# Performance work log

Measured on AMD Instinct MI355X. Metric: run time of the kernel, lower is better.

Reference implementation:

```python
import jax, jax.numpy as jnp
import numpy as np

B, S, H, NS, HEADS, L = 16, 1024, 1024, 32, 16, 5
DH = H // HEADS
LN_EPS = 1e-7


def setup_inputs() -> dict:
    key = jax.random.key(0)
    ks = jax.random.split(key, 12)
    std = 0.02
    inp = {
        "encoder_layer": jax.random.normal(ks[0], (B, S, H), jnp.float32),
        "lstm_W_ih": jax.random.normal(ks[1], (4 * H, H), jnp.float32) * std,
        "lstm_W_hh": jax.random.normal(ks[2], (4 * H, H), jnp.float32) * std,
        "lstm_b_ih": jnp.zeros((4 * H,), jnp.float32),
        "lstm_b_hh": jnp.zeros((4 * H,), jnp.float32),
        "ln_gamma": jnp.ones((H,), jnp.float32),
        "ln_beta": jnp.zeros((H,), jnp.float32),
        "Wq": jax.random.normal(ks[3], (H, H), jnp.float32) * std,
        "bq": jnp.zeros((H,), jnp.float32),
        "Wk": jax.random.normal(ks[4], (H, H), jnp.float32) * std,
        "bk": jnp.zeros((H,), jnp.float32),
        "Wv": jax.random.normal(ks[5], (H, H), jnp.float32) * std,
        "bv": jnp.zeros((H,), jnp.float32),
        "Wo": jax.random.normal(ks[6], (H, H), jnp.float32) * std,
        "bo": jnp.zeros((H,), jnp.float32),
        "attn_ln_gamma": jnp.ones((H,), jnp.float32),
        "attn_ln_beta": jnp.zeros((H,), jnp.float32),
        "clf_W": jax.random.normal(ks[7], (L, H), jnp.float32) * std,
        "clf_b": jnp.zeros((L,), jnp.float32),
    }
    # contiguous ragged spans: head_j = 32*j, tail_j = 32*(j+1); slice is head+1:tail
    seg = S // NS
    heads = jnp.tile(jnp.arange(NS, dtype=jnp.int32)[None, :] * seg, (B, 1))
    inp["span_head_idxs"] = heads
    inp["span_tail_idxs"] = heads + seg
    inp["span_attention_mask"] = jnp.ones((B, NS), jnp.int32)
    return inp


def _layer_norm(x, gamma, beta):
    mu = jnp.mean(x, axis=-1, keepdims=True)
    var = jnp.mean(jnp.square(x - mu), axis=-1, keepdims=True)
    return (x - mu) * jax.lax.rsqrt(var + LN_EPS) * gamma + beta


def reference(encoder_layer, lstm_W_ih, lstm_W_hh, lstm_b_ih, lstm_b_hh,
              ln_gamma, ln_beta, Wq, bq, Wk, bk, Wv, bv, Wo, bo,
              attn_ln_gamma, attn_ln_beta, clf_W, clf_b,
              span_head_idxs, span_tail_idxs, span_attention_mask):
    # --- unidirectional LSTM over the sequence (torch gate order i,f,g,o) ---
    x_tbh = jnp.swapaxes(encoder_layer, 0, 1)  # [S,B,H]
    h0 = jnp.zeros((B, H), encoder_layer.dtype)
    c0 = jnp.zeros((B, H), encoder_layer.dtype)

    def step(carry, xt):
        h, c = carry
        gates = xt @ lstm_W_ih.T + lstm_b_ih + h @ lstm_W_hh.T + lstm_b_hh
        i, f, g, o = jnp.split(gates, 4, axis=-1)
        i, f, o = jax.nn.sigmoid(i), jax.nn.sigmoid(f), jax.nn.sigmoid(o)
        c = f * c + i * jnp.tanh(g)
        h = o * jnp.tanh(c)
        return (h, c), h

    _, hs = jax.lax.scan(step, (h0, c0), x_tbh)
    enc = jnp.swapaxes(hs, 0, 1)  # [B,S,H]

    # --- ragged span mean pooling (tokens head+1 .. tail-1) via masked matmul ---
    t = jnp.arange(S, dtype=jnp.int32)  # [S]
    span_mask = ((t[None, None, :] >= span_head_idxs[:, :, None] + 1)
                 & (t[None, None, :] < span_tail_idxs[:, :, None]))  # [B,NS,S]
    mf = span_mask.astype(enc.dtype)
    sums = jnp.einsum('bns,bsh->bnh', mf, enc)
    counts = jnp.sum(mf, axis=-1, keepdims=True)
    mean_vec = sums / counts  # [B,NS,H]

    mean_vec = _layer_norm(mean_vec, ln_gamma, ln_beta)

    # --- DeBERTa-style self-attention (relative_attention=False) over spans ---
    m2d = (span_attention_mask[:, None, None, :]
           * span_attention_mask[:, None, :, None])  # [B,1,NS,NS]
    mbool = m2d.astype(bool)

    def split_heads(y):
        return jnp.swapaxes(y.reshape(B, NS, HEADS, DH), 1, 2)  # [B,h,NS,dh]

    q = split_heads(mean_vec @ Wq.T + bq)
    k = split_heads(mean_vec @ Wk.T + bk)
    v = split_heads(mean_vec @ Wv.T + bv)
    scale = jnp.sqrt(jnp.asarray(DH, mean_vec.dtype))
    scores = jnp.einsum('bhqd,bhkd->bhqk', q, k) / scale
    scores = jnp.where(mbool, scores, jnp.finfo(scores.dtype).min)
    probs = jax.nn.softmax(scores, axis=-1)
    probs = jnp.where(mbool, probs, 0.0)  # XSoftmax zeroes masked positions
    ctx = jnp.einsum('bhqk,bhkd->bhqd', probs, v)
    ctx = jnp.swapaxes(ctx, 1, 2).reshape(B, NS, H)
    attn_out = _layer_norm(ctx @ Wo.T + bo + mean_vec, attn_ln_gamma, attn_ln_beta)

    # dropout is identity in eval mode
    logits = attn_out @ clf_W.T + clf_b  # [B,NS,L]
    return logits
```

## Files before the change

kernel.cpp:

```cpp
#include <hip/hip_runtime.h>
#include <hip/hip_bf16.h>

#define DEV __device__ __forceinline__

typedef __attribute__((ext_vector_type(8))) short short8;
typedef __attribute__((ext_vector_type(4))) float f32x4;
typedef __attribute__((ext_vector_type(4))) unsigned int u32x4;

static constexpr int B_ = 16, S_ = 1024, H_ = 1024, NS_ = 32, HEADS_ = 16, L_ = 5;
static constexpr int G4H = 4096;
static constexpr int LSTM_GRID = 64;

DEV unsigned short f2bf(float f){
  union { float f; unsigned int i; } u; u.f = f;
  unsigned int r = (u.i + 0x7fffu + ((u.i >> 16) & 1u)) >> 16;
  return (unsigned short)r;
}
DEV float bf2f(unsigned short h){
  union { unsigned int i; float f; } u; u.i = ((unsigned int)h) << 16;
  return u.f;
}
DEV float sigm(float x){ return 1.f / (1.f + __expf(-x)); }
DEV float tanh_(float x){
  x = fminf(30.f, fmaxf(-30.f, x));
  float e = __expf(-2.f * x);
  return (1.f - e) / (1.f + e);
}

DEV u32x4 load_coh16(const void* p){
  u32x4 r;
  asm volatile("global_load_dwordx4 %0, %1, off sc0 sc1" : "=v"(r) : "v"(p));
  return r;
}
DEV void store_coh16(void* p, u32x4 v){
  asm volatile("global_store_dwordx4 %0, %1, off sc0 sc1" :: "v"(p), "v"(v) : "memory");
}

__global__ void k_spanof(const int* __restrict__ head, const int* __restrict__ tail,
                         int* __restrict__ spanof){
  const int b = blockIdx.x;
  for (int t = threadIdx.x; t < S_; t += blockDim.x) spanof[b * S_ + t] = -1;
  __syncthreads();
  if (threadIdx.x < NS_){
    const int n = threadIdx.x;
    const int h = head[b * NS_ + n], tl = tail[b * NS_ + n];
    for (int t = h + 1; t < tl; ++t) spanof[b * S_ + t] = n;
  }
}

__global__ __launch_bounds__(256) void k_gates(const float* __restrict__ enc,
    const float* __restrict__ Wih, const float* __restrict__ bih,
    const float* __restrict__ bhh, unsigned short* __restrict__ gx){
  const int nb = blockIdx.x;
  const int mb = blockIdx.y;
  __shared__ __align__(16) unsigned short As[128 * 40];
  __shared__ __align__(16) unsigned short Bs[128 * 40];
  const int tid = threadIdx.x, w = tid >> 6, l = tid & 63;
  const int wm = (w >> 1) * 64, wn = (w & 1) * 64;
  const int cl = l & 15, bg = l >> 4;
  f32x4 acc[4][4] = {};
  const int t0 = mb * 8, n0 = nb * 128;
  const int srow = tid >> 1, skq = (tid & 1) * 16;
  const int sb = srow & 15, stt = t0 + (srow >> 4);
  const float* Asrc = enc + ((size_t)sb * S_ + stt) * H_ + skq;
  const float* Bsrc = Wih + (size_t)(n0 + srow) * H_ + skq;
  for (int k0 = 0; k0 < H_; k0 += 32){
    #pragma unroll
    for (int q = 0; q < 4; ++q){
      float4 a = *(const float4*)(Asrc + k0 + q * 4);
      float4 b = *(const float4*)(Bsrc + k0 + q * 4);
      ushort4 ua; ua.x = f2bf(a.x); ua.y = f2bf(a.y); ua.z = f2bf(a.z); ua.w = f2bf(a.w);
      ushort4 ub; ub.x = f2bf(b.x); ub.y = f2bf(b.y); ub.z = f2bf(b.z); ub.w = f2bf(b.w);
      *(ushort4*)(As + srow * 40 + skq + q * 4) = ua;
      *(ushort4*)(Bs + srow * 40 + skq + q * 4) = ub;
    }
    __syncthreads();
    short8 af[4], bf[4];
    const int kq = bg * 8;
    #pragma unroll
    for (int i = 0; i < 4; ++i) af[i] = *(const short8*)(As + (wm + i * 16 + cl) * 40 + kq);
    #pragma unroll
    for (int i = 0; i < 4; ++i) bf[i] = *(const short8*)(Bs + (wn + i * 16 + cl) * 40 + kq);
    #pragma unroll
    for (int mi = 0; mi < 4; ++mi)
      #pragma unroll
      for (int ni = 0; ni < 4; ++ni)
        acc[mi][ni] = __builtin_amdgcn_mfma_f32_16x16x32_bf16(af[mi], bf[ni], acc[mi][ni], 0, 0, 0);
    __syncthreads();
  }
  #pragma unroll
  for (int ni = 0; ni < 4; ++ni){
    const int c = n0 + wn + ni * 16 + cl;
    const float bias = bih[c] + bhh[c];
    const int g = c >> 10, j = c & 1023;
    const int cuq = j >> 4, wq = (j >> 2) & 3, jjq = j & 3;
    const int nq = jjq * 4 + g;
    #pragma unroll
    for (int mi = 0; mi < 4; ++mi){
      const int tg = t0 + ((wm + mi * 16) >> 4);
      ushort4 o;
      o.x = f2bf(acc[mi][ni].x + bias);
      o.y = f2bf(acc[mi][ni].y + bias);
      o.z = f2bf(acc[mi][ni].z + bias);
      o.w = f2bf(acc[mi][ni].w + bias);
      const size_t u4i = (((size_t)tg * 64 + cuq) * 64 + (wq * 16 + nq)) * 4 + bg;
      *((ushort4*)gx + u4i) = o;
    }
  }
}

__global__ __launch_bounds__(256, 1) void k_lstm(const float* __restrict__ Whh,
    const unsigned short* __restrict__ gx, const int* __restrict__ spanof,
    unsigned short* __restrict__ hbuf, float* __restrict__ sums,
    unsigned int* __restrict__ bar){
  extern __shared__ unsigned char smem[];
  unsigned char* Wl = smem;
  unsigned char* Hl = smem + 131072;
  unsigned short* Hs = (unsigned short*)Hl;
  const int cu = blockIdx.x, tid = threadIdx.x;
  const int w = tid >> 6, l = tid & 63;

  {
    const int r = tid >> 2, kq = (tid & 3) * 256;
    const int rn = r & 15, rw = r >> 4;
    const int rg = rn & 3, rjj = rn >> 2;
    const int rj = cu * 16 + rw * 4 + rjj;
    const float* src = Whh + (size_t)(rg * H_ + rj) * H_ + kq;
    for (int k = 0; k < 256; k += 4){
      float4 v = *(const float4*)(src + k);
      ushort4 u; u.x = f2bf(v.x); u.y = f2bf(v.y); u.z = f2bf(v.z); u.w = f2bf(v.w);
      unsigned int a = (unsigned)(r * 2048 + (kq + k) * 2);
      a ^= (unsigned)((r & 7) << 4);
      *(ushort4*)(Wl + a) = u;
    }
  }
  __syncthreads();

  const int n = l & 15, bg = l >> 4;
  const int g = n & 3, jj = n >> 2;
  const int j = cu * 16 + w * 4 + jj;
  const int bstar = bg * 4 + g;
  const int jl = w * 4 + jj;

  const unsigned int abase = (unsigned)(n * 2048 + bg * 16);
  const unsigned int aswz  = (unsigned)((n & 7) << 4);
  const int wrow = w * 16 + n;
  const unsigned int bbase = (unsigned)(wrow * 2048 + bg * 16);
  const unsigned int bswz  = (unsigned)((wrow & 7) << 4);

  const ushort4* gxp = (const ushort4*)gx + ((size_t)cu * 64 + w * 16 + n) * 4 + bg;
  const int* sp = spanof + (size_t)bstar * S_;

  float cstate = 0.f, pool = 0.f;
  int curspan = -1;

  for (int t = 0; t < S_; ++t){
    const int p = t & 1;
    const ushort4 gxv = gxp[(size_t)t * 16384];
    const int s = sp[t];
    {
      const unsigned char* hsrc = (const unsigned char*)hbuf + p * 32768 + w * 8192 + l * 16;
      u32x4 v0 = load_coh16(hsrc + 0 * 1024);
      u32x4 v1 = load_coh16(hsrc + 1 * 1024);
      u32x4 v2 = load_coh16(hsrc + 2 * 1024);
      u32x4 v3 = load_coh16(hsrc + 3 * 1024);
      u32x4 v4 = load_coh16(hsrc + 4 * 1024);
      u32x4 v5 = load_coh16(hsrc + 5 * 1024);
      u32x4 v6 = load_coh16(hsrc + 6 * 1024);
      u32x4 v7 = load_coh16(hsrc + 7 * 1024);
      asm volatile("s_waitcnt vmcnt(0)" ::: "memory");
      __builtin_amdgcn_sched_barrier(0);
      unsigned char* hdst = Hl + w * 8192 + l * 16;
      *(u32x4*)(hdst + 0 * 1024) = v0;
      *(u32x4*)(hdst + 1 * 1024) = v1;
      *(u32x4*)(hdst + 2 * 1024) = v2;
      *(u32x4*)(hdst + 3 * 1024) = v3;
      *(u32x4*)(hdst + 4 * 1024) = v4;
      *(u32x4*)(hdst + 5 * 1024) = v5;
      *(u32x4*)(hdst + 6 * 1024) = v6;
      *(u32x4*)(hdst + 7 * 1024) = v7;
    }
    __syncthreads();
    f32x4 a0 = {0,0,0,0}, a1 = {0,0,0,0}, a2 = {0,0,0,0}, a3 = {0,0,0,0};
    #pragma unroll
    for (int kk = 0; kk < 32; kk += 4){
      short8 h0 = *(const short8*)(Hl + ((abase + (kk + 0) * 64) ^ aswz));
      short8 w0 = *(const short8*)(Wl + ((bbase + (kk + 0) * 64) ^ bswz));
      a0 = __builtin_amdgcn_mfma_f32_16x16x32_bf16(h0, w0, a0, 0, 0, 0);
      short8 h1 = *(const short8*)(Hl + ((abase + (kk + 1) * 64) ^ aswz));
      short8 w1 = *(const short8*)(Wl + ((bbase + (kk + 1) * 64) ^ bswz));
      a1 = __builtin_amdgcn_mfma_f32_16x16x32_bf16(h1, w1, a1, 0, 0, 0);
      short8 h2 = *(const short8*)(Hl + ((abase + (kk + 2) * 64) ^ aswz));
      short8 w2 = *(const short8*)(Wl + ((bbase + (kk + 2) * 64) ^ bswz));
      a2 = __builtin_amdgcn_mfma_f32_16x16x32_bf16(h2, w2, a2, 0, 0, 0);
      short8 h3 = *(const short8*)(Hl + ((abase + (kk + 3) * 64) ^ aswz));
      short8 w3 = *(const short8*)(Wl + ((bbase + (kk + 3) * 64) ^ bswz));
      a3 = __builtin_amdgcn_mfma_f32_16x16x32_bf16(h3, w3, a3, 0, 0, 0);
    }
    f32x4 acc = (a0 + a1) + (a2 + a3);
    const float x0 = acc.x + bf2f(gxv.x);
    const float x1 = acc.y + bf2f(gxv.y);
    const float x2 = acc.z + bf2f(gxv.z);
    const float x3 = acc.w + bf2f(gxv.w);
    const float s1 = (g==0)?x1:(g==1)?x0:(g==2)?x3:x2;
    const float s2 = (g==0)?x2:(g==1)?x3:(g==2)?x0:x1;
    const float s3 = (g==0)?x3:(g==1)?x2:(g==2)?x1:x0;
    const float r1 = __shfl_xor(s1, 1, 64);
    const float r2 = __shfl_xor(s2, 2, 64);
    const float r3 = __shfl_xor(s3, 3, 64);
    const float own = (g==0)?x0:(g==1)?x1:(g==2)?x2:x3;
    const float vi = (g==0)?own:(g==1)?r1:(g==2)?r2:r3;
    const float vf = (g==1)?own:(g==0)?r1:(g==3)?r2:r3;
    const float vg = (g==2)?own:(g==3)?r1:(g==0)?r2:r3;
    const float vo = (g==3)?own:(g==2)?r1:(g==1)?r2:r3;
    const float ig = sigm(vi), fg = sigm(vf), gt = tanh_(vg), og = sigm(vo);
    cstate = fg * cstate + ig * gt;
    const float hval = og * tanh_(cstate);
    if (s != curspan){
      if (curspan >= 0) sums[((size_t)bstar * NS_ + curspan) * H_ + j] = pool;
      pool = 0.f; curspan = s;
    }
    if (s >= 0) pool += hval;
    __syncthreads();
    Hs[bstar * 16 + jl] = f2bf(hval);
    __syncthreads();
    if (tid < 32){
      const int sb = tid >> 1, half = tid & 1;
      const unsigned key = (unsigned)((sb & 7) << 4);
      const unsigned off = (unsigned)(sb * 2048)
          + ((unsigned)(cu * 32) ^ (key & 0x60))
          + ((unsigned)(half * 16) ^ (key & 0x10));
      u32x4 v = *(const u32x4*)((const unsigned char*)Hl + tid * 16);
      store_coh16((unsigned char*)hbuf + (p ^ 1) * 32768 + off, v);
    }
    if (tid == 0){
      asm volatile("s_waitcnt vmcnt(0)" ::: "memory");
      __hip_atomic_fetch_add(bar, 1u, __ATOMIC_RELAXED, __HIP_MEMORY_SCOPE_AGENT);
      const unsigned int want = (unsigned)(t + 1) * LSTM_GRID;
      int guard = 0;
      while (__hip_atomic_load(bar, __ATOMIC_RELAXED, __HIP_MEMORY_SCOPE_AGENT) < want){
        __builtin_amdgcn_s_sleep(1);
        if (++guard > 4000000) break;
      }
    }
    __syncthreads();
  }
  if (curspan >= 0) sums[((size_t)bstar * NS_ + curspan) * H_ + j] = pool;
}

DEV float block_sum(float v, float* red, int tid){
  #pragma unroll
  for (int d = 1; d < 64; d <<= 1) v += __shfl_xor(v, d, 64);
  if ((tid & 63) == 0) red[tid >> 6] = v;
  __syncthreads();
  const float r = red[0] + red[1] + red[2] + red[3];
  __syncthreads();
  return r;
}

__global__ __launch_bounds__(256) void k_poolln(const float* __restrict__ sums,
    const int* __restrict__ head, const int* __restrict__ tail,
    const float* __restrict__ gamma, const float* __restrict__ beta,
    unsigned short* __restrict__ mvb, float* __restrict__ mvf){
  __shared__ float red[4];
  const int m = blockIdx.x, tid = threadIdx.x;
  const float inv = 1.f / (float)(tail[m] - head[m] - 1);
  float4 x = *(const float4*)(sums + (size_t)m * H_ + tid * 4);
  x.x *= inv; x.y *= inv; x.z *= inv; x.w *= inv;
  const float mu = block_sum(x.x + x.y + x.z + x.w, red, tid) * (1.f / (float)H_);
  const float d0 = x.x - mu, d1 = x.y - mu, d2 = x.z - mu, d3 = x.w - mu;
  const float var = block_sum(d0*d0 + d1*d1 + d2*d2 + d3*d3, red, tid) * (1.f / (float)H_);
  const float rs = rsqrtf(var + 1e-7f);
  float4 gm = *(const float4*)(gamma + tid * 4);
  float4 bt = *(const float4*)(beta + tid * 4);
  float4 o; o.x = d0*rs*gm.x + bt.x; o.y = d1*rs*gm.y + bt.y;
  o.z = d2*rs*gm.z + bt.z; o.w = d3*rs*gm.w + bt.w;
  *(float4*)(mvf + (size_t)m * H_ + tid * 4) = o;
  ushort4 u; u.x = f2bf(o.x); u.y = f2bf(o.y); u.z = f2bf(o.z); u.w = f2bf(o.w);
  *(ushort4*)(mvb + (size_t)m * H_ + tid * 4) = u;
}

template<int OUT_BF16>
__global__ __launch_bounds__(256) void k_gemm2(const unsigned short* __restrict__ A,
    const float* __restrict__ Bw, const float* __restrict__ bias,
    float* __restrict__ Cf, unsigned short* __restrict__ Cb, int Nn){
  const int nb = blockIdx.x, mb = blockIdx.y;
  __shared__ __align__(16) unsigned short As[128 * 40];
  __shared__ __align__(16) unsigned short Bs[128 * 40];
  const int tid = threadIdx.x, w = tid >> 6, l = tid & 63;
  const int wm = (w >> 1) * 64, wn = (w & 1) * 64;
  const int cl = l & 15, bg = l >> 4;
  f32x4 acc[4][4] = {};
  const int m0 = mb * 128, n0 = nb * 128;
  const int srow = tid >> 1, skq = (tid & 1) * 16;
  const unsigned short* Asrc = A + (size_t)(m0 + srow) * 1024 + skq;
  const float* Bsrc = Bw + (size_t)(n0 + srow) * 1024 + skq;
  for (int k0 = 0; k0 < 1024; k0 += 32){
    uint4 av0 = *(const uint4*)(Asrc + k0);
    uint4 av1 = *(const uint4*)(Asrc + k0 + 8);
    *(uint4*)(As + srow * 40 + skq) = av0;
    *(uint4*)(As + srow * 40 + skq + 8) = av1;
    #pragma unroll
    for (int q = 0; q < 4; ++q){
      float4 b = *(const float4*)(Bsrc + k0 + q * 4);
      ushort4 ub; ub.x = f2bf(b.x); ub.y = f2bf(b.y); ub.z = f2bf(b.z); ub.w = f2bf(b.w);
      *(ushort4*)(Bs + srow * 40 + skq + q * 4) = ub;
    }
    __syncthreads();
    short8 af[4], bf[4];
    const int kq = bg * 8;
    #pragma unroll
    for (int i = 0; i < 4; ++i) af[i] = *(const short8*)(As + (wm + i * 16 + cl) * 40 + kq);
    #pragma unroll
    for (int i = 0; i < 4; ++i) bf[i] = *(const short8*)(Bs + (wn + i * 16 + cl) * 40 + kq);
    #pragma unroll
    for (int mi = 0; mi < 4; ++mi)
      #pragma unroll
      for (int ni = 0; ni < 4; ++ni)
        acc[mi][ni] = __builtin_amdgcn_mfma_f32_16x16x32_bf16(af[mi], bf[ni], acc[mi][ni], 0, 0, 0);
    __syncthreads();
  }
  #pragma unroll
  for (int ni = 0; ni < 4; ++ni){
    const int c = n0 + wn + ni * 16 + cl;
    const float bsv = bias ? bias[c] : 0.f;
    #pragma unroll
    for (int mi = 0; mi < 4; ++mi){
      const int m = m0 + wm + mi * 16 + bg * 4;
      const float v0 = acc[mi][ni].x + bsv, v1 = acc[mi][ni].y + bsv;
      const float v2 = acc[mi][ni].z + bsv, v3 = acc[mi][ni].w + bsv;
      if (OUT_BF16){
        Cb[(size_t)(m + 0) * Nn + c] = f2bf(v0);
        Cb[(size_t)(m + 1) * Nn + c] = f2bf(v1);
        Cb[(size_t)(m + 2) * Nn + c] = f2bf(v2);
        Cb[(size_t)(m + 3) * Nn + c] = f2bf(v3);
      } else {
        Cf[(size_t)(m + 0) * Nn + c] = v0;
        Cf[(size_t)(m + 1) * Nn + c] = v1;
        Cf[(size_t)(m + 2) * Nn + c] = v2;
        Cf[(size_t)(m + 3) * Nn + c] = v3;
      }
    }
  }
}

__global__ __launch_bounds__(256) void k_attn(const unsigned short* __restrict__ qb,
    const unsigned short* __restrict__ kb, const unsigned short* __restrict__ vb,
    const int* __restrict__ mask, unsigned short* __restrict__ ctx){
  const int bh = blockIdx.x, b = bh >> 4, hd = bh & 15;
  __shared__ float Q[32][64], K[32][64], V[32][64], Sc[32][33];
  __shared__ int msk[32];
  const int tid = threadIdx.x;
  const int row = tid >> 3, d0 = (tid & 7) * 8;
  {
    const size_t base = (size_t)(b * NS_ + row) * H_ + hd * 64 + d0;
    uint4 vq = *(const uint4*)(qb + base);
    uint4 vk = *(const uint4*)(kb + base);
    uint4 vv = *(const uint4*)(vb + base);
    const unsigned int wq[4] = {vq.x, vq.y, vq.z, vq.w};
    const unsigned int wk[4] = {vk.x, vk.y, vk.z, vk.w};
    const unsigned int wv[4] = {vv.x, vv.y, vv.z, vv.w};
    #pragma unroll
    for (int i = 0; i < 4; ++i){
      Q[row][d0 + 2*i]     = bf2f((unsigned short)(wq[i] & 0xffff));
      Q[row][d0 + 2*i + 1] = bf2f((unsigned short)(wq[i] >> 16));
      K[row][d0 + 2*i]     = bf2f((unsigned short)(wk[i] & 0xffff));
      K[row][d0 + 2*i + 1] = bf2f((unsigned short)(wk[i] >> 16));
      V[row][d0 + 2*i]     = bf2f((unsigned short)(wv[i] & 0xffff));
      V[row][d0 + 2*i + 1] = bf2f((unsigned short)(wv[i] >> 16));
    }
  }
  if (tid < 32) msk[tid] = mask[b * NS_ + tid];
  __syncthreads();
  {
    const int qi = tid >> 3, kb0 = (tid & 7) * 4;
    for (int kk = kb0; kk < kb0 + 4; ++kk){
      float s = 0.f;
      #pragma unroll
      for (int d = 0; d < 64; ++d) s += Q[qi][d] * K[kk][d];
      s *= 0.125f;
      if (!msk[qi] || !msk[kk]) s = -3.402823466e38f;
      Sc[qi][kk] = s;
    }
  }
  __syncthreads();
  if (tid < 32){
    float mx = -3.402823466e38f;
    for (int kk = 0; kk < 32; ++kk) mx = fmaxf(mx, Sc[tid][kk]);
    float sum = 0.f;
    for (int kk = 0; kk < 32; ++kk){
      const float e = __expf(Sc[tid][kk] - mx);
      Sc[tid][kk] = e; sum += e;
    }
    const float isum = 1.f / sum;
    for (int kk = 0; kk < 32; ++kk){
      float pv = Sc[tid][kk] * isum;
      if (!msk[tid] || !msk[kk]) pv = 0.f;
      Sc[tid][kk] = pv;
    }
  }
  __syncthreads();
  float o[8] = {0,0,0,0,0,0,0,0};
  for (int kk = 0; kk < 32; ++kk){
    const float p = Sc[row][kk];
    #pragma unroll
    for (int i = 0; i < 8; ++i) o[i] += p * V[kk][d0 + i];
  }
  ushort4 oA, oB;
  oA.x = f2bf(o[0]); oA.y = f2bf(o[1]); oA.z = f2bf(o[2]); oA.w = f2bf(o[3]);
  oB.x = f2bf(o[4]); oB.y = f2bf(o[5]); oB.z = f2bf(o[6]); oB.w = f2bf(o[7]);
  unsigned short* cp = ctx + (size_t)(b * NS_ + row) * H_ + hd * 64 + d0;
  *(ushort4*)(cp) = oA;
  *(ushort4*)(cp + 4) = oB;
}

__global__ __launch_bounds__(256) void k_residln(const float* __restrict__ wo,
    const float* __restrict__ mvf, const float* __restrict__ gamma,
    const float* __restrict__ beta, float* __restrict__ aof){
  __shared__ float red[4];
  const int m = blockIdx.x, tid = threadIdx.x;
  float4 a = *(const float4*)(wo + (size_t)m * H_ + tid * 4);
  float4 r = *(const float4*)(mvf + (size_t)m * H_ + tid * 4);
  float4 x; x.x = a.x + r.x; x.y = a.y + r.y; x.z = a.z + r.z; x.w = a.w + r.w;
  const float mu = block_sum(x.x + x.y + x.z + x.w, red, tid) * (1.f / (float)H_);
  const float d0 = x.x - mu, d1 = x.y - mu, d2 = x.z - mu, d3 = x.w - mu;
  const float var = block_sum(d0*d0 + d1*d1 + d2*d2 + d3*d3, red, tid) * (1.f / (float)H_);
  const float rs = rsqrtf(var + 1e-7f);
  float4 gm = *(const float4*)(gamma + tid * 4);
  float4 bt = *(const float4*)(beta + tid * 4);
  float4 o; o.x = d0*rs*gm.x + bt.x; o.y = d1*rs*gm.y + bt.y;
  o.z = d2*rs*gm.z + bt.z; o.w = d3*rs*gm.w + bt.w;
  *(float4*)(aof + (size_t)m * H_ + tid * 4) = o;
}

__global__ __launch_bounds__(64) void k_clf(const float* __restrict__ ao,
    const float* __restrict__ Wc, const float* __restrict__ bc, float* __restrict__ out){
  const int m = blockIdx.x, l = threadIdx.x;
  const float* a = ao + (size_t)m * H_ + l * 16;
  float av[16];
  #pragma unroll
  for (int i = 0; i < 4; ++i){
    float4 v = *(const float4*)(a + i * 4);
    av[i*4+0] = v.x; av[i*4+1] = v.y; av[i*4+2] = v.z; av[i*4+3] = v.w;
  }
  float p[5];
  #pragma unroll
  for (int c = 0; c < 5; ++c){
    const float* wr = Wc + (size_t)c * H_ + l * 16;
    float s = 0.f;
    #pragma unroll
    for (int i = 0; i < 4; ++i){
      float4 v = *(const float4*)(wr + i * 4);
      s += av[i*4+0]*v.x + av[i*4+1]*v.y + av[i*4+2]*v.z + av[i*4+3]*v.w;
    }
    p[c] = s;
  }
  #pragma unroll
  for (int d = 1; d < 64; d <<= 1){
    #pragma unroll
    for (int c = 0; c < 5; ++c) p[c] += __shfl_xor(p[c], d, 64);
  }
  if (l == 0){
    #pragma unroll
    for (int c = 0; c < 5; ++c) out[m * L_ + c] = p[c] + bc[c];
  }
}

extern "C" void kernel_launch(void* const* d_in, const int* in_sizes, int n_in,
                              void* d_out, int out_size, void* d_ws, size_t ws_size,
                              hipStream_t stream){
  (void)in_sizes; (void)n_in; (void)out_size; (void)ws_size;
  const float* enc  = (const float*)d_in[0];
  const float* Wih  = (const float*)d_in[1];
  const float* Whh  = (const float*)d_in[2];
  const float* bih  = (const float*)d_in[3];
  const float* bhh  = (const float*)d_in[4];
  const float* lng  = (const float*)d_in[5];
  const float* lnb  = (const float*)d_in[6];
  const float* Wq   = (const float*)d_in[7];
  const float* bq   = (const float*)d_in[8];
  const float* Wk   = (const float*)d_in[9];
  const float* bk   = (const float*)d_in[10];
  const float* Wv   = (const float*)d_in[11];
  const float* bv   = (const float*)d_in[12];
  const float* Wo   = (const float*)d_in[13];
  const float* bo   = (const float*)d_in[14];
  const float* alng = (const float*)d_in[15];
  const float* alnb = (const float*)d_in[16];
  const float* clfW = (const float*)d_in[17];
  const float* clfb = (const float*)d_in[18];
  const int* shead  = (const int*)d_in[19];
  const int* stail  = (const int*)d_in[20];
  const int* smask  = (const int*)d_in[21];
  float* out = (float*)d_out;
  unsigned char* ws = (unsigned char*)d_ws;

  size_t cur = 0;
  auto alloc = [&](size_t sz){ size_t r = cur; cur = (cur + sz + 255) & ~(size_t)255; return r; };
  const size_t off_gx   = alloc((size_t)S_ * G4H * B_ * 2);
  const size_t off_hbuf = alloc(2 * (size_t)B_ * H_ * 2);
  const size_t off_bar  = alloc(256);
  const size_t off_span = alloc((size_t)B_ * S_ * 4);
  const size_t off_sums = alloc((size_t)B_ * NS_ * H_ * 4);
  const size_t off_mvb  = alloc((size_t)B_ * NS_ * H_ * 2);
  const size_t off_mvf  = alloc((size_t)B_ * NS_ * H_ * 4);
  const size_t off_q    = alloc((size_t)B_ * NS_ * H_ * 2);
  const size_t off_k    = alloc((size_t)B_ * NS_ * H_ * 2);
  const size_t off_v    = alloc((size_t)B_ * NS_ * H_ * 2);
  const size_t off_ctx  = alloc((size_t)B_ * NS_ * H_ * 2);
  const size_t off_wo   = alloc((size_t)B_ * NS_ * H_ * 4);
  const size_t off_ao   = alloc((size_t)B_ * NS_ * H_ * 4);

  unsigned short* gx   = (unsigned short*)(ws + off_gx);
  unsigned short* hbuf = (unsigned short*)(ws + off_hbuf);
  unsigned int*   bar  = (unsigned int*)(ws + off_bar);
  int*            span = (int*)(ws + off_span);
  float*          sums = (float*)(ws + off_sums);
  unsigned short* mvb  = (unsigned short*)(ws + off_mvb);
  float*          mvf  = (float*)(ws + off_mvf);
  unsigned short* qb   = (unsigned short*)(ws + off_q);
  unsigned short* kbp  = (unsigned short*)(ws + off_k);
  unsigned short* vbp  = (unsigned short*)(ws + off_v);
  unsigned short* ctx  = (unsigned short*)(ws + off_ctx);
  float*          wob  = (float*)(ws + off_wo);
  float*          aof  = (float*)(ws + off_ao);

  (void)hipMemsetAsync(hbuf, 0, 2 * (size_t)B_ * H_ * 2, stream);
  (void)hipMemsetAsync(bar, 0, 256, stream);
  (void)hipMemsetAsync(sums, 0, (size_t)B_ * NS_ * H_ * 4, stream);

  k_spanof<<<B_, 256, 0, stream>>>(shead, stail, span);
  k_gates<<<dim3(32, 128), 256, 0, stream>>>(enc, Wih, bih, bhh, gx);

  (void)hipFuncSetAttribute((const void*)k_lstm,
      hipFuncAttributeMaxDynamicSharedMemorySize, 163840);
  k_lstm<<<LSTM_GRID, 256, 163840, stream>>>(Whh, gx, span, hbuf, sums, bar);

  k_poolln<<<B_ * NS_, 256, 0, stream>>>(sums, shead, stail, lng, lnb, mvb, mvf);
  k_gemm2<1><<<dim3(8, 4), 256, 0, stream>>>(mvb, Wq, bq, nullptr, qb, 1024);
  k_gemm2<1><<<dim3(8, 4), 256, 0, stream>>>(mvb, Wk, bk, nullptr, kbp, 1024);
  k_gemm2<1><<<dim3(8, 4), 256, 0, stream>>>(mvb, Wv, bv, nullptr, vbp, 1024);
  k_attn<<<B_ * HEADS_, 256, 0, stream>>>(qb, kbp, vbp, smask, ctx);
  k_gemm2<0><<<dim3(8, 4), 256, 0, stream>>>(ctx, Wo, bo, wob, nullptr, 1024);
  k_residln<<<B_ * NS_, 256, 0, stream>>>(wob, mvf, alng, alnb, aof);
  k_clf<<<B_ * NS_, 64, 0, stream>>>(aof, clfW, clfb, out);
}
```

Measured before the change: 4.529 ms.

## Keep LSTM recurrent weights in registers and replace grid barrier with per-block tags

The persistent LSTM kernel now holds its slice of W_hh as bf16 MFMA operands in VGPRs instead of LDS. Each wave loads the full hidden state straight from global memory into registers, with no LDS staging or block-wide syncs. The global atomic-counter barrier is replaced by per-block step tags that consumers poll with a wave-wide all-check, so a block waits only for the tags to show the current step rather than for a counter. The intent is to take LDS round-trips and barrier latency off the serial per-timestep critical path. The cost is very high register pressure, 32 short8 weights plus 32 short8 hidden values per lane, and 4x more global hidden-state loads per block; it also relies on relaxed atomics for cross-block ordering.

New measurement: 6.400 ms. 41.3% more time.

```diff
diff --git a/kernel.cpp b/kernel.cpp
--- a/kernel.cpp
+++ b/kernel.cpp
@@ -27,8 +27,8 @@
   return (1.f - e) / (1.f + e);
 }
 
-DEV u32x4 load_coh16(const void* p){
-  u32x4 r;
+DEV short8 load_coh16(const void* p){
+  short8 r;
   asm volatile("global_load_dwordx4 %0, %1, off sc0 sc1" : "=v"(r) : "v"(p));
   return r;
 }
@@ -111,42 +111,32 @@
 
 __global__ __launch_bounds__(256, 1) void k_lstm(const float* __restrict__ Whh,
     const unsigned short* __restrict__ gx, const int* __restrict__ spanof,
-    unsigned short* __restrict__ hbuf, float* __restrict__ sums,
-    unsigned int* __restrict__ bar){
-  extern __shared__ unsigned char smem[];
-  unsigned char* Wl = smem;
-  unsigned char* Hl = smem + 131072;
-  unsigned short* Hs = (unsigned short*)Hl;
+    unsigned short* __restrict__ hbuf, unsigned int* __restrict__ tags,
+    float* __restrict__ sums){
+  __shared__ __align__(16) unsigned short Hs[256];
   const int cu = blockIdx.x, tid = threadIdx.x;
   const int w = tid >> 6, l = tid & 63;
-
-  {
-    const int r = tid >> 2, kq = (tid & 3) * 256;
-    const int rn = r & 15, rw = r >> 4;
-    const int rg = rn & 3, rjj = rn >> 2;
-    const int rj = cu * 16 + rw * 4 + rjj;
-    const float* src = Whh + (size_t)(rg * H_ + rj) * H_ + kq;
-    for (int k = 0; k < 256; k += 4){
-      float4 v = *(const float4*)(src + k);
-      ushort4 u; u.x = f2bf(v.x); u.y = f2bf(v.y); u.z = f2bf(v.z); u.w = f2bf(v.w);
-      unsigned int a = (unsigned)(r * 2048 + (kq + k) * 2);
-      a ^= (unsigned)((r & 7) << 4);
-      *(ushort4*)(Wl + a) = u;
-    }
-  }
-  __syncthreads();
-
   const int n = l & 15, bg = l >> 4;
   const int g = n & 3, jj = n >> 2;
   const int j = cu * 16 + w * 4 + jj;
   const int bstar = bg * 4 + g;
   const int jl = w * 4 + jj;
 
-  const unsigned int abase = (unsigned)(n * 2048 + bg * 16);
-  const unsigned int aswz  = (unsigned)((n & 7) << 4);
-  const int wrow = w * 16 + n;
-  const unsigned int bbase = (unsigned)(wrow * 2048 + bg * 16);
-  const unsigned int bswz  = (unsigned)((wrow & 7) << 4);
+  short8 wr[32];
+  {
+    const float* ws = Whh + (size_t)(g * H_ + j) * H_ + bg * 8;
+    #pragma unroll
+    for (int kk = 0; kk < 32; ++kk){
+      float4 x = *(const float4*)(ws + kk * 32);
+      float4 y = *(const float4*)(ws + kk * 32 + 4);
+      short8 v;
+      v[0] = (short)f2bf(x.x); v[1] = (short)f2bf(x.y);
+      v[2] = (short)f2bf(x.z); v[3] = (short)f2bf(x.w);
+      v[4] = (short)f2bf(y.x); v[5] = (short)f2bf(y.y);
+      v[6] = (short)f2bf(y.z); v[7] = (short)f2bf(y.w);
+      wr[kk] = v;
+    }
+  }
 
   const ushort4* gxp = (const ushort4*)gx + ((size_t)cu * 64 + w * 16 + n) * 4 + bg;
   const int* sp = spanof + (size_t)bstar * S_;
@@ -159,43 +149,30 @@
     const ushort4 gxv = gxp[(size_t)t * 16384];
     const int s = sp[t];
     {
-      const unsigned char* hsrc = (const unsigned char*)hbuf + p * 32768 + w * 8192 + l * 16;
-      u32x4 v0 = load_coh16(hsrc + 0 * 1024);
-      u32x4 v1 = load_coh16(hsrc + 1 * 1024);
-      u32x4 v2 = load_coh16(hsrc + 2 * 1024);
-      u32x4 v3 = load_coh16(hsrc + 3 * 1024);
-      u32x4 v4 = load_coh16(hsrc + 4 * 1024);
-      u32x4 v5 = load_coh16(hsrc + 5 * 1024);
-      u32x4 v6 = load_coh16(hsrc + 6 * 1024);
-      u32x4 v7 = load_coh16(hsrc + 7 * 1024);
+      const unsigned int* tp = tags + (size_t)p * 1024 + (size_t)l * 16;
+      unsigned int v = __hip_atomic_load(tp, __ATOMIC_RELAXED, __HIP_MEMORY_SCOPE_AGENT);
+      int guard = 0;
+      while (!__all(v == (unsigned int)t)){
+        __builtin_amdgcn_s_sleep(1);
+        v = __hip_atomic_load(tp, __ATOMIC_RELAXED, __HIP_MEMORY_SCOPE_AGENT);
+        if (++guard > 2000000) break;
+      }
+    }
+    short8 hv[32];
+    {
+      const unsigned char* hb = (const unsigned char*)hbuf + p * 32768 + n * 2048 + bg * 16;
+      #pragma unroll
+      for (int kk = 0; kk < 32; ++kk) hv[kk] = load_coh16(hb + kk * 64);
       asm volatile("s_waitcnt vmcnt(0)" ::: "memory");
       __builtin_amdgcn_sched_barrier(0);
-      unsigned char* hdst = Hl + w * 8192 + l * 16;
-      *(u32x4*)(hdst + 0 * 1024) = v0;
-      *(u32x4*)(hdst + 1 * 1024) = v1;
-      *(u32x4*)(hdst + 2 * 1024) = v2;
-      *(u32x4*)(hdst + 3 * 1024) = v3;
-      *(u32x4*)(hdst + 4 * 1024) = v4;
-      *(u32x4*)(hdst + 5 * 1024) = v5;
-      *(u32x4*)(hdst + 6 * 1024) = v6;
-      *(u32x4*)(hdst + 7 * 1024) = v7;
-    }
-    __syncthreads();
+    }
     f32x4 a0 = {0,0,0,0}, a1 = {0,0,0,0}, a2 = {0,0,0,0}, a3 = {0,0,0,0};
     #pragma unroll
     for (int kk = 0; kk < 32; kk += 4){
-      short8 h0 = *(const short8*)(Hl + ((abase + (kk + 0) * 64) ^ aswz));
-      short8 w0 = *(const short8*)(Wl + ((bbase + (kk + 0) * 64) ^ bswz));
-      a0 = __builtin_amdgcn_mfma_f32_16x16x32_bf16(h0, w0, a0, 0, 0, 0);
-      short8 h1 = *(const short8*)(Hl + ((abase + (kk + 1) * 64) ^ aswz));
-      short8 w1 = *(const short8*)(Wl + ((bbase + (kk + 1) * 64) ^ bswz));
-      a1 = __builtin_amdgcn_mfma_f32_16x16x32_bf16(h1, w1, a1, 0, 0, 0);
-      short8 h2 = *(const short8*)(Hl + ((abase + (kk + 2) * 64) ^ aswz));
-      short8 w2 = *(const short8*)(Wl + ((bbase + (kk + 2) * 64) ^ bswz));
-      a2 = __builtin_amdgcn_mfma_f32_16x16x32_bf16(h2, w2, a2, 0, 0, 0);
-      short8 h3 = *(const short8*)(Hl + ((abase + (kk + 3) * 64) ^ aswz));
-      short8 w3 = *(const short8*)(Wl + ((bbase + (kk + 3) * 64) ^ bswz));
-      a3 = __builtin_amdgcn_mfma_f32_16x16x32_bf16(h3, w3, a3, 0, 0, 0);
+      a0 = __builtin_amdgcn_mfma_f32_16x16x32_bf16(hv[kk + 0], wr[kk + 0], a0, 0, 0, 0);
+      a1 = __builtin_amdgcn_mfma_f32_16x16x32_bf16(hv[kk + 1], wr[kk + 1], a1, 0, 0, 0);
+      a2 = __builtin_amdgcn_mfma_f32_16x16x32_bf16(hv[kk + 2], wr[kk + 2], a2, 0, 0, 0);
+      a3 = __builtin_amdgcn_mfma_f32_16x16x32_bf16(hv[kk + 3], wr[kk + 3], a3, 0, 0, 0);
     }
     f32x4 acc = (a0 + a1) + (a2 + a3);
     const float x0 = acc.x + bf2f(gxv.x);
@@ -221,29 +198,18 @@
       pool = 0.f; curspan = s;
     }
     if (s >= 0) pool += hval;
-    __syncthreads();
     Hs[bstar * 16 + jl] = f2bf(hval);
     __syncthreads();
     if (tid < 32){
       const int sb = tid >> 1, half = tid & 1;
-      const unsigned key = (unsigned)((sb & 7) << 4);
-      const unsigned off = (unsigned)(sb * 2048)
-          + ((unsigned)(cu * 32) ^ (key & 0x60))
-          + ((unsigned)(half * 16) ^ (key & 0x10));
-      u32x4 v = *(const u32x4*)((const unsigned char*)Hl + tid * 16);
-      store_coh16((unsigned char*)hbuf + (p ^ 1) * 32768 + off, v);
+      u32x4 v = *(const u32x4*)((const unsigned char*)Hs + tid * 16);
+      store_coh16((unsigned char*)hbuf + (p ^ 1) * 32768 + sb * 2048 + cu * 32 + half * 16, v);
     }
     if (tid == 0){
       asm volatile("s_waitcnt vmcnt(0)" ::: "memory");
-      __hip_atomic_fetch_add(bar, 1u, __ATOMIC_RELAXED, __HIP_MEMORY_SCOPE_AGENT);
-      const unsigned int want = (unsigned)(t + 1) * LSTM_GRID;
-      int guard = 0;
-      while (__hip_atomic_load(bar, __ATOMIC_RELAXED, __HIP_MEMORY_SCOPE_AGENT) < want){
-        __builtin_amdgcn_s_sleep(1);
-        if (++guard > 4000000) break;
-      }
-    }
-    __syncthreads();
+      __hip_atomic_store(tags + (size_t)((t + 1) & 1) * 1024 + (size_t)cu * 16,
+                         (unsigned int)(t + 1), __ATOMIC_RELAXED, __HIP_MEMORY_SCOPE_AGENT);
+    }
   }
   if (curspan >= 0) sums[((size_t)bstar * NS_ + curspan) * H_ + j] = pool;
 }
@@ -499,7 +465,7 @@
   auto alloc = [&](size_t sz){ size_t r = cur; cur = (cur + sz + 255) & ~(size_t)255; return r; };
   const size_t off_gx   = alloc((size_t)S_ * G4H * B_ * 2);
   const size_t off_hbuf = alloc(2 * (size_t)B_ * H_ * 2);
-  const size_t off_bar  = alloc(256);
+  const size_t off_tags = alloc(2 * 1024 * 4);
   const size_t off_span = alloc((size_t)B_ * S_ * 4);
   const size_t off_sums = alloc((size_t)B_ * NS_ * H_ * 4);
   const size_t off_mvb  = alloc((size_t)B_ * NS_ * H_ * 2);
@@ -513,7 +479,7 @@
 
   unsigned short* gx   = (unsigned short*)(ws + off_gx);
   unsigned short* hbuf = (unsigned short*)(ws + off_hbuf);
-  unsigned int*   bar  = (unsigned int*)(ws + off_bar);
+  unsigned int*   tags = (unsigned int*)(ws + off_tags);
   int*            span = (int*)(ws + off_span);
   float*          sums = (float*)(ws + off_sums);
   unsigned short* mvb  = (unsigned short*)(ws + off_mvb);
@@ -526,15 +492,13 @@
   float*          aof  = (float*)(ws + off_ao);
 
   (void)hipMemsetAsync(hbuf, 0, 2 * (size_t)B_ * H_ * 2, stream);
-  (void)hipMemsetAsync(bar, 0, 256, stream);
+  (void)hipMemsetAsync(tags, 0, 2 * 1024 * 4, stream);
   (void)hipMemsetAsync(sums, 0, (size_t)B_ * NS_ * H_ * 4, stream);
 
   k_spanof<<<B_, 256, 0, stream>>>(shead, stail, span);
   k_gates<<<dim3(32, 128), 256, 0, stream>>>(enc, Wih, bih, bhh, gx);
 
-  (void)hipFuncSetAttribute((const void*)k_lstm,
-      hipFuncAttributeMaxDynamicSharedMemorySize, 163840);
-  k_lstm<<<LSTM_GRID, 256, 163840, stream>>>(Whh, gx, span, hbuf, sums, bar);
+  k_lstm<<<LSTM_GRID, 256, 0, stream>>>(Whh, gx, span, hbuf, tags, sums);
 
   k_poolln<<<B_ * NS_, 256, 0, stream>>>(sums, shead, stail, lng, lnb, mvb, mvf);
   k_gemm2<1><<<dim3(8, 4), 256, 0, stream>>>(mvb, Wq, bq, nullptr, qb, 1024);
```
